# Kernel tuning notes

Measured on AMD Instinct MI355X. Metric: run time of the kernel, lower is better.

## Reference

```python
import jax, jax.numpy as jnp
import numpy as np

NUM_HEADS = 16
ROPE_BASE = 10000.0
NEG_INF = float('-inf')


def _rotate_half_interleaved(x):
    # x: [..., d]; interleaved rotation: (-x2, x1) pairs
    x1 = x[..., ::2]
    x2 = x[..., 1::2]
    return jnp.stack((-x2, x1), axis=-1).reshape(x.shape)


def _rope_tables(seq_len, head_dim, dtype):
    inv_freq = 1.0 / (ROPE_BASE ** (jnp.arange(0, head_dim, 2, dtype=jnp.float32) / head_dim))
    pos = jnp.arange(seq_len, dtype=jnp.float32)
    freqs = pos[:, None] * inv_freq[None, :]          # [S, d/2]
    emb = jnp.concatenate((freqs, freqs), axis=-1)    # [S, d]  (HF-style concat, as in source)
    return jnp.cos(emb).astype(dtype), jnp.sin(emb).astype(dtype)


def setup_inputs() -> dict:
    key = jax.random.key(0)
    ks = jax.random.split(key, 4)
    B, S, H = 2, 2048, 2048
    scale = 0.02
    x = jax.random.normal(ks[0], (B, S, H), dtype=jnp.float32)
    qkv_w = jax.random.normal(ks[1], (3 * H, H), dtype=jnp.float32) * scale
    qkv_b = jnp.zeros((3 * H,), dtype=jnp.float32)
    out_w = jax.random.normal(ks[2], (H, H), dtype=jnp.float32) * scale
    out_b = jnp.zeros((H,), dtype=jnp.float32)
    attention_mask = jnp.ones((B, S), dtype=jnp.int32)
    return {"x": x, "attention_mask": attention_mask, "qkv_w": qkv_w,
            "qkv_b": qkv_b, "out_w": out_w, "out_b": out_b}


def reference(x, attention_mask, qkv_w, qkv_b, out_w, out_b):
    B, S, H = x.shape
    nh = NUM_HEADS
    hd = H // nh
    scale = hd ** -0.5

    qkv = x @ qkv_w.T + qkv_b                            # [B,S,3H]
    qkv = qkv.reshape(B, S, 3, nh, hd).transpose(2, 0, 3, 1, 4)  # [3,B,nh,S,hd]
    q, k, v = qkv[0], qkv[1], qkv[2]

    cos, sin = _rope_tables(S, hd, x.dtype)              # [S,hd]
    cos = cos[None, None, :, :]
    sin = sin[None, None, :, :]
    q = q * cos + _rotate_half_interleaved(q) * sin
    k = k * cos + _rotate_half_interleaved(k) * sin

    scores = jnp.einsum('bhqd,bhkd->bhqk', q, k) * scale  # [B,nh,S,S]
    causal = jnp.triu(jnp.ones((S, S), dtype=bool), k=1)
    scores = jnp.where(causal[None, None], NEG_INF, scores)
    key_mask = (attention_mask == 0)[:, None, None, :]    # [B,1,1,S]
    scores = jnp.where(key_mask, NEG_INF, scores)

    weights = jax.nn.softmax(scores, axis=-1)
    attn = jnp.einsum('bhqk,bhkd->bhqd', weights, v)       # [B,nh,S,hd]
    attn = attn.transpose(0, 2, 1, 3).reshape(B, S, H)
    return attn @ out_w.T + out_b
```

## Files before the change

kernel.cpp:

```cpp
#include <hip/hip_runtime.h>

typedef __bf16 bf16;
typedef __bf16 bf16x4 __attribute__((ext_vector_type(4)));
typedef __bf16 bf16x8 __attribute__((ext_vector_type(8)));
typedef float f32x4 __attribute__((ext_vector_type(4)));
typedef float f32x16 __attribute__((ext_vector_type(16)));

#define MFMA_BF16(a, b, c) __builtin_amdgcn_mfma_f32_16x16x32_bf16(a, b, c, 0, 0, 0)
#define MFMA32(a, b, c)    __builtin_amdgcn_mfma_f32_32x32x16_bf16(a, b, c, 0, 0, 0)

__device__ __forceinline__ void async16(const void* g, void* l) {
    __builtin_amdgcn_global_load_lds(
        (const __attribute__((address_space(1))) void*)g,
        (__attribute__((address_space(3))) void*)l,
        16, 0, 0);
}

__global__ void cvt8(const float* __restrict__ in, bf16* __restrict__ out, int n) {
    int i = (blockIdx.x * 256 + threadIdx.x) * 8;
    if (i >= n) return;
    float4 a = *(const float4*)(in + i);
    float4 b = *(const float4*)(in + i + 4);
    bf16x8 o;
    o[0] = (bf16)a.x; o[1] = (bf16)a.y; o[2] = (bf16)a.z; o[3] = (bf16)a.w;
    o[4] = (bf16)b.x; o[5] = (bf16)b.y; o[6] = (bf16)b.z; o[7] = (bf16)b.w;
    *(bf16x8*)(out + i) = o;
}

__global__ void tables_k(const int* __restrict__ am, float* __restrict__ cosT,
                         float* __restrict__ sinT, float* __restrict__ mbias) {
    int i = blockIdx.x * 256 + threadIdx.x;
    int s = i >> 7, d = i & 127, fi = d & 63;
    float inv = exp2f(-(float)fi * (13.287712379549449f / 64.0f));
    float ang = (float)s * inv;
    cosT[i] = cosf(ang);
    sinT[i] = sinf(ang);
    if (i < 2 * 2048) mbias[i] = (am[i] == 0) ? -1e30f : 0.0f;
}

template <int EPI>
__global__ void __launch_bounds__(256, 2)
gemm_bt(const bf16* __restrict__ A, const bf16* __restrict__ Bt,
        const float* __restrict__ bias, float* __restrict__ Cf,
        bf16* __restrict__ qb, bf16* __restrict__ kb, bf16* __restrict__ vtb,
        const float* __restrict__ cosT, const float* __restrict__ sinT,
        int M, int N, int K) {
    __shared__ __align__(16) bf16 sA[128 * 64];
    __shared__ __align__(16) bf16 sB[128 * 64];
    const int tid  = threadIdx.x;
    const int lane = tid & 63;
    const int quad = lane >> 4, l15 = lane & 15;
    const int wid = tid >> 6, wm = wid >> 1, wn = wid & 1;
    const int bm = blockIdx.x, bn = blockIdx.y;

    f32x4 acc[4][4];
#pragma unroll
    for (int i = 0; i < 4; i++)
#pragma unroll
        for (int j = 0; j < 4; j++)
#pragma unroll
            for (int c = 0; c < 4; c++) acc[i][j][c] = 0.0f;

    const int r0 = tid >> 3, x0 = tid & 7;
    const int g0 = x0 ^ (r0 & 7);
    const bf16* pa = A  + (size_t)(bm * 128 + r0) * K + g0 * 8;
    const bf16* pb = Bt + (size_t)(bn * 128 + r0) * K + g0 * 8;
    bf16* la = sA + tid * 8;
    bf16* lb = sB + tid * 8;
    const size_t gstep = (size_t)32 * K;

    for (int k0 = 0; k0 < K; k0 += 64) {
#pragma unroll
        for (int i = 0; i < 4; i++) {
            async16(pa + i * gstep, la + i * 2048);
            async16(pb + i * gstep, lb + i * 2048);
        }
        pa += 64; pb += 64;
        __syncthreads();
#pragma unroll
        for (int ks = 0; ks < 2; ks++) {
            bf16x8 af[4], bfr[4];
#pragma unroll
            for (int i = 0; i < 4; i++) {
                int r = wm * 64 + i * 16 + l15;
                int x = (ks * 4 + quad) ^ (r & 7);
                af[i] = *(const bf16x8*)(sA + r * 64 + x * 8);
            }
#pragma unroll
            for (int i = 0; i < 4; i++) {
                int r = wn * 64 + i * 16 + l15;
                int x = (ks * 4 + quad) ^ (r & 7);
                bfr[i] = *(const bf16x8*)(sB + r * 64 + x * 8);
            }
#pragma unroll
            for (int mi = 0; mi < 4; mi++)
#pragma unroll
                for (int ni = 0; ni < 4; ni++)
                    acc[mi][ni] = MFMA_BF16(af[mi], bfr[ni], acc[mi][ni]);
        }
        __syncthreads();
    }

    if (EPI == 0) {
#pragma unroll
        for (int mi = 0; mi < 4; mi++)
#pragma unroll
            for (int ni = 0; ni < 4; ni++) {
                int row0 = bm * 128 + wm * 64 + mi * 16 + quad * 4;
                int col  = bn * 128 + wn * 64 + ni * 16 + l15;
                float bv = bias[col];
#pragma unroll
                for (int r = 0; r < 4; r++)
                    Cf[(size_t)(row0 + r) * N + col] = acc[mi][ni][r] + bv;
            }
    } else {
#pragma unroll
        for (int mi = 0; mi < 4; mi++)
#pragma unroll
            for (int ni = 0; ni < 4; ni++) {
                int col   = bn * 128 + wn * 64 + ni * 16 + l15;
                int which = col >> 11;
                int hcol  = col & 2047;
                int h = hcol >> 7, d = hcol & 127;
                float bv = bias[col];
#pragma unroll
                for (int r = 0; r < 4; r++) {
                    int row = bm * 128 + wm * 64 + mi * 16 + quad * 4 + r;
                    int b = row >> 11, s = row & 2047;
                    float v  = acc[mi][ni][r] + bv;
                    float vp = __shfl_xor(v, 1, 64);
                    float ov = v;
                    if (which < 2) {
                        float c  = cosT[(s << 7) + d];
                        float sn = sinT[(s << 7) + d];
                        ov = v * c + ((d & 1) ? vp : -vp) * sn;
                    }
                    if (which == 0) ov *= 0.08838834764831845f;
                    size_t bh = (size_t)(b * 16 + h);
                    if (which == 0)      qb[(bh * 2048 + s) * 128 + d] = (bf16)ov;
                    else if (which == 1) kb[(bh * 2048 + s) * 128 + d] = (bf16)ov;
                    else                 vtb[(bh * 128 + d) * 2048 + s] = (bf16)ov;
                }
            }
    }
}

__global__ void __launch_bounds__(256, 2)
fattn(const bf16* __restrict__ Q, const bf16* __restrict__ Kg,
      const bf16* __restrict__ Vt, const float* __restrict__ mbias,
      bf16* __restrict__ O) {
    __shared__ __align__(16) bf16 sK[64 * 128];
    __shared__ __align__(16) bf16 sV[128 * 64];
    __shared__ __align__(16) bf16 sP[4 * 32 * 64];
    const int tid = threadIdx.x, lane = tid & 63, w = tid >> 6;
    const int l31 = lane & 31, half = lane >> 5;
    const int bx = (int)blockIdx.x;
    const int qt = (bx & 1) ? 15 - (bx >> 1) : (bx >> 1);
    const int bh = blockIdx.y, b = bh >> 4, hh = bh & 15;
    const int myq = qt * 128 + w * 32 + l31;

    const bf16* Qb  = Q  + (size_t)bh * 2048 * 128;
    const bf16* Kbh = Kg + (size_t)bh * 2048 * 128;
    const bf16* Vbh = Vt + (size_t)bh * 128 * 2048;
    const float* mbb = mbias + b * 2048;
    bf16* sPw = sP + w * 2048;

    bf16x8 qf[8];
#pragma unroll
    for (int kq = 0; kq < 8; kq++)
        qf[kq] = *(const bf16x8*)(Qb + (size_t)myq * 128 + kq * 16 + half * 8);

    f32x16 oacc[4];
#pragma unroll
    for (int dt = 0; dt < 4; dt++)
#pragma unroll
        for (int c = 0; c < 16; c++) oacc[dt][c] = 0.0f;
    float m_s = -3e38f, l_s = 0.0f;

    const int rk = tid >> 4, xk = tid & 15, gk = xk ^ (rk & 15);
    const int rv = tid >> 3, xv = tid & 7,  gv = xv ^ (rv & 7);
    const int nkt = 2 * qt + 2;

    for (int kt = 0; kt < nkt; kt++) {
        const int kb0 = kt * 64;
#pragma unroll
        for (int i = 0; i < 4; i++) {
            async16(Kbh + (size_t)(kb0 + rk + i * 16) * 128 + gk * 8, sK + (i * 256 + tid) * 8);
            async16(Vbh + (size_t)(rv + i * 32) * 2048 + kb0 + gv * 8, sV + (i * 256 + tid) * 8);
        }
        __syncthreads();

        f32x16 sacc[2];
#pragma unroll
        for (int t = 0; t < 2; t++)
#pragma unroll
            for (int c = 0; c < 16; c++) sacc[t][c] = 0.0f;
#pragma unroll
        for (int kq = 0; kq < 8; kq++) {
#pragma unroll
            for (int t = 0; t < 2; t++) {
                int row = t * 32 + l31;
                int x = (kq * 2 + half) ^ (row & 15);
                bf16x8 kf = *(const bf16x8*)(sK + row * 128 + x * 8);
                sacc[t] = MFMA32(kf, qf[kq], sacc[t]);
            }
        }

        float ps[2][16];
        float mx = -3e38f;
#pragma unroll
        for (int t = 0; t < 2; t++)
#pragma unroll
            for (int g = 0; g < 4; g++) {
                float4 mb4 = *(const float4*)(mbb + kb0 + t * 32 + 8 * g + 4 * half);
#pragma unroll
                for (int r2 = 0; r2 < 4; r2++) {
                    int sk = kb0 + t * 32 + 8 * g + 4 * half + r2;
                    float v = sacc[t][g * 4 + r2] + ((const float*)&mb4)[r2];
                    v = (sk > myq) ? -1e30f : v;
                    ps[t][g * 4 + r2] = v;
                    mx = fmaxf(mx, v);
                }
            }

        mx = fmaxf(mx, __shfl_xor(mx, 32, 64));
        float mnew  = fmaxf(m_s, mx);
        float alpha = __expf(m_s - mnew);
        float rs = 0.0f;
#pragma unroll
        for (int t = 0; t < 2; t++)
#pragma unroll
            for (int c = 0; c < 16; c++) {
                float p = __expf(ps[t][c] - mnew);
                ps[t][c] = p;
                rs += p;
            }
        rs += __shfl_xor(rs, 32, 64);
        l_s = l_s * alpha + rs;
        m_s = mnew;
#pragma unroll
        for (int dt = 0; dt < 4; dt++) oacc[dt] *= alpha;

#pragma unroll
        for (int t = 0; t < 2; t++)
#pragma unroll
            for (int g = 0; g < 4; g++) {
                int c = t * 4 + g;
                int x = c ^ (l31 & 7);
                bf16x4 p4;
#pragma unroll
                for (int r2 = 0; r2 < 4; r2++) p4[r2] = (bf16)ps[t][g * 4 + r2];
                *(bf16x4*)(sPw + l31 * 64 + x * 8 + half * 4) = p4;
            }

#pragma unroll
        for (int kq2 = 0; kq2 < 4; kq2++) {
            int cp = kq2 * 2 + half;
            int xp = cp ^ (l31 & 7);
            bf16x8 pf = *(const bf16x8*)(sPw + l31 * 64 + xp * 8);
#pragma unroll
            for (int dt = 0; dt < 4; dt++) {
                int row = dt * 32 + l31;
                int xv2 = cp ^ (row & 7);
                bf16x8 vf = *(const bf16x8*)(sV + row * 64 + xv2 * 8);
                oacc[dt] = MFMA32(vf, pf, oacc[dt]);
            }
        }
        __syncthreads();
    }

    float inv = 1.0f / l_s;
    size_t base = ((size_t)(b * 2048 + myq)) * 2048 + hh * 128;
#pragma unroll
    for (int dt = 0; dt < 4; dt++)
#pragma unroll
        for (int g = 0; g < 4; g++) {
            bf16x4 o4;
#pragma unroll
            for (int r2 = 0; r2 < 4; r2++) o4[r2] = (bf16)(oacc[dt][g * 4 + r2] * inv);
            *(bf16x4*)(O + base + dt * 32 + 8 * g + 4 * half) = o4;
        }
}

extern "C" void kernel_launch(void* const* d_in, const int* in_sizes, int n_in,
                              void* d_out, int out_size, void* d_ws, size_t ws_size,
                              hipStream_t stream) {
    const float* x     = (const float*)d_in[0];
    const int*   am    = (const int*)d_in[1];
    const float* qkvw  = (const float*)d_in[2];
    const float* qkvb  = (const float*)d_in[3];
    const float* outw  = (const float*)d_in[4];
    const float* outb  = (const float*)d_in[5];
    float* out = (float*)d_out;

    char* ws = (char*)d_ws;
    bf16*  xb    = (bf16*)(ws);
    bf16*  wqkv  = (bf16*)(ws + (16ull << 20));
    bf16*  wout  = (bf16*)(ws + (40ull << 20));
    bf16*  qb    = (bf16*)(ws + (48ull << 20));
    bf16*  kb    = (bf16*)(ws + (64ull << 20));
    bf16*  vtb   = (bf16*)(ws + (80ull << 20));
    bf16*  attn  = (bf16*)(ws + (96ull << 20));
    float* cosT  = (float*)(ws + (112ull << 20));
    float* sinT  = (float*)(ws + (113ull << 20));
    float* mbias = (float*)(ws + (114ull << 20));

    cvt8<<<4096, 256, 0, stream>>>(x, xb, 4096 * 2048);
    cvt8<<<6144, 256, 0, stream>>>(qkvw, wqkv, 6144 * 2048);
    cvt8<<<2048, 256, 0, stream>>>(outw, wout, 2048 * 2048);
    tables_k<<<1024, 256, 0, stream>>>(am, cosT, sinT, mbias);

    gemm_bt<1><<<dim3(32, 48), 256, 0, stream>>>(
        xb, wqkv, qkvb, nullptr, qb, kb, vtb, cosT, sinT, 4096, 6144, 2048);

    fattn<<<dim3(16, 32), 256, 0, stream>>>(qb, kb, vtb, mbias, attn);

    gemm_bt<0><<<dim3(32, 16), 256, 0, stream>>>(
        attn, wout, outb, out, nullptr, nullptr, nullptr, nullptr, nullptr,
        4096, 2048, 2048);
}
```

Measured before the change: 413.4 us.

## Double-buffer K/V tiles in flash attention and split QKV GEMM launch

The attention kernel now prefetches the next K/V tile into a second LDS buffer while computing on the current one, so global loads overlap with MFMA work. The per-tile cross-half row-sum shuffle moves to a single shuffle after the loop. The QKV GEMM is split into two launches of half the column blocks each via a new column-offset argument. Double buffering doubles K/V LDS use, which may lower occupancy. The wait for async loads relies on the trailing barrier, which may not guarantee the prefetched data has landed.

After: 409.0 us. No clear change (-1.1%).

```diff
diff --git a/kernel.cpp b/kernel.cpp
--- a/kernel.cpp
+++ b/kernel.cpp
@@ -44,14 +44,14 @@
         const float* __restrict__ bias, float* __restrict__ Cf,
         bf16* __restrict__ qb, bf16* __restrict__ kb, bf16* __restrict__ vtb,
         const float* __restrict__ cosT, const float* __restrict__ sinT,
-        int M, int N, int K) {
+        int M, int N, int K, int bn0) {
     __shared__ __align__(16) bf16 sA[128 * 64];
     __shared__ __align__(16) bf16 sB[128 * 64];
     const int tid  = threadIdx.x;
     const int lane = tid & 63;
     const int quad = lane >> 4, l15 = lane & 15;
     const int wid = tid >> 6, wm = wid >> 1, wn = wid & 1;
-    const int bm = blockIdx.x, bn = blockIdx.y;
+    const int bm = blockIdx.x, bn = blockIdx.y + bn0;
 
     f32x4 acc[4][4];
 #pragma unroll
@@ -149,8 +149,8 @@
 fattn(const bf16* __restrict__ Q, const bf16* __restrict__ Kg,
       const bf16* __restrict__ Vt, const float* __restrict__ mbias,
       bf16* __restrict__ O) {
-    __shared__ __align__(16) bf16 sK[64 * 128];
-    __shared__ __align__(16) bf16 sV[128 * 64];
+    __shared__ __align__(16) bf16 sK[2][64 * 128];
+    __shared__ __align__(16) bf16 sV[2][128 * 64];
     __shared__ __align__(16) bf16 sP[4 * 32 * 64];
     const int tid = threadIdx.x, lane = tid & 63, w = tid >> 6;
     const int l31 = lane & 31, half = lane >> 5;
@@ -181,14 +181,28 @@
     const int rv = tid >> 3, xv = tid & 7,  gv = xv ^ (rv & 7);
     const int nkt = 2 * qt + 2;
 
+#pragma unroll
+    for (int i = 0; i < 4; i++) {
+        async16(Kbh + (size_t)(rk + i * 16) * 128 + gk * 8, &sK[0][(i * 256 + tid) * 8]);
+        async16(Vbh + (size_t)(rv + i * 32) * 2048 + gv * 8, &sV[0][(i * 256 + tid) * 8]);
+    }
+    __syncthreads();
+
     for (int kt = 0; kt < nkt; kt++) {
         const int kb0 = kt * 64;
-#pragma unroll
-        for (int i = 0; i < 4; i++) {
-            async16(Kbh + (size_t)(kb0 + rk + i * 16) * 128 + gk * 8, sK + (i * 256 + tid) * 8);
-            async16(Vbh + (size_t)(rv + i * 32) * 2048 + kb0 + gv * 8, sV + (i * 256 + tid) * 8);
-        }
-        __syncthreads();
+        const int buf = kt & 1;
+        if (kt + 1 < nkt) {
+            const int nb0 = kb0 + 64;
+#pragma unroll
+            for (int i = 0; i < 4; i++) {
+                async16(Kbh + (size_t)(nb0 + rk + i * 16) * 128 + gk * 8,
+                        &sK[buf ^ 1][(i * 256 + tid) * 8]);
+                async16(Vbh + (size_t)(rv + i * 32) * 2048 + nb0 + gv * 8,
+                        &sV[buf ^ 1][(i * 256 + tid) * 8]);
+            }
+        }
+        const bf16* sKb = sK[buf];
+        const bf16* sVb = sV[buf];
 
         f32x16 sacc[2];
 #pragma unroll
@@ -201,7 +215,7 @@
             for (int t = 0; t < 2; t++) {
                 int row = t * 32 + l31;
                 int x = (kq * 2 + half) ^ (row & 15);
-                bf16x8 kf = *(const bf16x8*)(sK + row * 128 + x * 8);
+                bf16x8 kf = *(const bf16x8*)(sKb + row * 128 + x * 8);
                 sacc[t] = MFMA32(kf, qf[kq], sacc[t]);
             }
         }
@@ -235,7 +249,6 @@
                 ps[t][c] = p;
                 rs += p;
             }
-        rs += __shfl_xor(rs, 32, 64);
         l_s = l_s * alpha + rs;
         m_s = mnew;
 #pragma unroll
@@ -262,13 +275,14 @@
             for (int dt = 0; dt < 4; dt++) {
                 int row = dt * 32 + l31;
                 int xv2 = cp ^ (row & 7);
-                bf16x8 vf = *(const bf16x8*)(sV + row * 64 + xv2 * 8);
+                bf16x8 vf = *(const bf16x8*)(sVb + row * 64 + xv2 * 8);
                 oacc[dt] = MFMA32(vf, pf, oacc[dt]);
             }
         }
         __syncthreads();
     }
 
+    l_s += __shfl_xor(l_s, 32, 64);
     float inv = 1.0f / l_s;
     size_t base = ((size_t)(b * 2048 + myq)) * 2048 + hh * 128;
 #pragma unroll
@@ -310,12 +324,14 @@
     cvt8<<<2048, 256, 0, stream>>>(outw, wout, 2048 * 2048);
     tables_k<<<1024, 256, 0, stream>>>(am, cosT, sinT, mbias);
 
-    gemm_bt<1><<<dim3(32, 48), 256, 0, stream>>>(
-        xb, wqkv, qkvb, nullptr, qb, kb, vtb, cosT, sinT, 4096, 6144, 2048);
+    gemm_bt<1><<<dim3(32, 24), 256, 0, stream>>>(
+        xb, wqkv, qkvb, nullptr, qb, kb, vtb, cosT, sinT, 4096, 6144, 2048, 0);
+    gemm_bt<1><<<dim3(32, 24), 256, 0, stream>>>(
+        xb, wqkv, qkvb, nullptr, qb, kb, vtb, cosT, sinT, 4096, 6144, 2048, 24);
 
     fattn<<<dim3(16, 32), 256, 0, stream>>>(qb, kb, vtb, mbias, attn);
 
     gemm_bt<0><<<dim3(32, 16), 256, 0, stream>>>(
         attn, wout, outb, out, nullptr, nullptr, nullptr, nullptr, nullptr,
-        4096, 2048, 2048);
-}
+        4096, 2048, 2048, 0);
+}
```
